# Performance work log

Measured on AMD Instinct MI355X. Metric: run time of the kernel, lower is better.

Reference implementation:

```python
import jax, jax.numpy as jnp
import numpy as np
from jax import lax

N = 1 << 22      # variable nodes
DV = 4           # max variable degree
M = 1 << 21      # check nodes
DC = 8           # max check degree
E = N * DV       # total edges (== M * DC, regular code)
N_ITER = 5


def setup_inputs() -> dict:
    key = jax.random.key(0)
    k1, k2 = jax.random.split(key)
    llr0 = jax.random.normal(k1, (N,), dtype=jnp.float32)
    # cn_adj: each check node owns DC flat edge indices into the [N, DV] grid
    perm = jax.random.permutation(k2, E)
    cn_adj = perm.reshape(M, DC).astype(jnp.int32)
    # vn_adj: only its sign is used (vn_adj < 0 masks padded slots); regular code -> no padding
    vn_adj = (jnp.arange(E, dtype=jnp.int32) % M).reshape(N, DV)
    gamma = jnp.ones((), dtype=jnp.float32)  # learned damping scalar
    return {"llr0": llr0, "gamma": gamma, "vn_adj": vn_adj, "cn_adj": cn_adj}


def reference(llr0, gamma, vn_adj, cn_adj):
    n, dv = vn_adj.shape
    mask = cn_adj < 0                       # [M, DC] padded check slots
    idx = jnp.where(mask, 0, cn_adj)        # safe flat edge indices
    vmask = vn_adj < 0                      # [N, DV] padded variable slots
    big = jnp.asarray(1e9, llr0.dtype)

    def step(v2c, _):
        # gather variable->check messages per check row: [M, DC]
        msg = v2c.reshape(-1)[idx]
        msg = jnp.where(mask, 0.0, msg)
        # min-sum check update (non-extrinsic, as in source)
        sgn = jnp.prod(jnp.sign(msg + 1e-12), axis=1, keepdims=True)   # [M, 1]
        mag = jnp.min(jnp.abs(jnp.where(mask, big, msg)), axis=1, keepdims=True)
        c2v = gamma * sgn * mag
        c2v = jnp.where(mask, 0.0, jnp.broadcast_to(c2v, cn_adj.shape))
        # scatter check->variable messages back onto the edge grid
        v_acc = jnp.zeros((n * dv,), v2c.dtype).at[idx].add(c2v).reshape(n, dv)
        v2c_new = llr0[:, None] + v_acc - v2c
        v2c_new = jnp.where(vmask, 0.0, v2c_new)
        return v2c_new, None

    v2c0 = jnp.zeros(vn_adj.shape, dtype=llr0.dtype)
    v2c, _ = lax.scan(step, v2c0, None, length=N_ITER)
    return llr0 + jnp.sum(v2c, axis=1)
```

## Files before the change

kernel.cpp:

```cpp
#include <hip/hip_runtime.h>
#include <hip/hip_bf16.h>

#define N_VAR (1 << 22)
#define DV    4
#define M_CHK (1 << 21)
#define DC    8
#define N_ITER 5
#define E_TOT (N_VAR * DV)

#define NBIN         256
#define REC_PER_BIN  (E_TOT / NBIN)
#define K3_BLOCKS    4096
#define CHK_PER_THR  2
#define CHK_PER_BLK  (M_CHK / K3_BLOCKS)
#define REC_PER_BLK  (CHK_PER_BLK * DC)
#define VARS_PER_BIN (N_VAR / NBIN)

typedef int      iv4 __attribute__((ext_vector_type(4)));
typedef unsigned uv4 __attribute__((ext_vector_type(4)));
typedef float    fv4 __attribute__((ext_vector_type(4)));

static __device__ inline unsigned pack_bf16x2(float lo, float hi) {
    float2 t; t.x = lo; t.y = hi;
    __hip_bfloat162 h = __float22bfloat162_rn(t);
    return *reinterpret_cast<unsigned*>(&h);
}

__global__ __launch_bounds__(256) void llr_to_bf16(const fv4* __restrict__ llr4,
                                                   uv4* __restrict__ out,
                                                   unsigned* __restrict__ gctr) {
    const int t = blockIdx.x * blockDim.x + threadIdx.x;
    if (blockIdx.x == 0) gctr[threadIdx.x] = 0u;
    fv4 a = __builtin_nontemporal_load(&llr4[(size_t)t * 2]);
    fv4 b = __builtin_nontemporal_load(&llr4[(size_t)t * 2 + 1]);
    uv4 o;
    o.x = pack_bf16x2(a.x, a.y);
    o.y = pack_bf16x2(a.z, a.w);
    o.z = pack_bf16x2(b.x, b.y);
    o.w = pack_bf16x2(b.z, b.w);
    __builtin_nontemporal_store(o, &out[t]);
}

__global__ __launch_bounds__(256) void k_emit(const __hip_bfloat16* __restrict__ llrb,
                                              const float* __restrict__ gamma_p,
                                              const iv4* __restrict__ cn_adj4,
                                              unsigned* __restrict__ gctr,
                                              unsigned* __restrict__ g_rec) {
    __shared__ unsigned hist[NBIN], binOfs[NBIN], cnt2[NBIN], gbase[NBIN], scanBuf[NBIN];
    __shared__ unsigned recLds[REC_PER_BLK];
    __shared__ unsigned char binLds[REC_PER_BLK];
    const int tid = threadIdx.x, blk = blockIdx.x;
    const float gamma = gamma_p[0];

    hist[tid] = 0;
    cnt2[tid] = 0;
    __syncthreads();

    int e[CHK_PER_THR][DC];
    const int m0 = blk * CHK_PER_BLK + tid * CHK_PER_THR;
#pragma unroll
    for (int c = 0; c < CHK_PER_THR; ++c) {
        iv4 a0 = __builtin_nontemporal_load(&cn_adj4[(size_t)(m0 + c) * 2]);
        iv4 a1 = __builtin_nontemporal_load(&cn_adj4[(size_t)(m0 + c) * 2 + 1]);
        e[c][0]=a0.x; e[c][1]=a0.y; e[c][2]=a0.z; e[c][3]=a0.w;
        e[c][4]=a1.x; e[c][5]=a1.y; e[c][6]=a1.z; e[c][7]=a1.w;
    }
    float l[CHK_PER_THR][DC];
#pragma unroll
    for (int c = 0; c < CHK_PER_THR; ++c)
#pragma unroll
        for (int d = 0; d < DC; ++d)
            l[c][d] = __bfloat162float(llrb[e[c][d] >> 2]);

    unsigned Sh[CHK_PER_THR];
#pragma unroll
    for (int c = 0; c < CHK_PER_THR; ++c) {
        float s1 = 1.0f, m1 = fabsf(l[c][0]);
#pragma unroll
        for (int d = 0; d < DC; ++d) {
            float t = l[c][d] + 1e-12f;
            s1 *= (t > 0.0f) ? 1.0f : ((t < 0.0f) ? -1.0f : 0.0f);
            if (d > 0) m1 = fminf(m1, fabsf(l[c][d]));
        }
        float c1 = gamma * s1 * m1;
        float delta = gamma * fabsf(c1) - c1;
        float s3 = 1.0f, m3 = fabsf(l[c][0] + delta);
#pragma unroll
        for (int d = 0; d < DC; ++d) {
            float ld = l[c][d] + delta;
            float t = ld + 1e-12f;
            s3 *= (t > 0.0f) ? 1.0f : ((t < 0.0f) ? -1.0f : 0.0f);
            if (d > 0) m3 = fminf(m3, fabsf(ld));
        }
        float c3 = gamma * s3 * m3;
        float c4 = gamma * fabsf(c3 - delta);
        float S  = (c4 - c3) + delta;
        __hip_bfloat16 h = __float2bfloat16(S);
        Sh[c] = *reinterpret_cast<unsigned short*>(&h);
    }

#pragma unroll
    for (int c = 0; c < CHK_PER_THR; ++c)
#pragma unroll
        for (int d = 0; d < DC; ++d)
            atomicAdd(&hist[(unsigned)e[c][d] >> 16], 1u);
    __syncthreads();

    scanBuf[tid] = hist[tid];
    __syncthreads();
    for (int d = 1; d < NBIN; d <<= 1) {
        unsigned t = (tid >= d) ? scanBuf[tid - d] : 0u;
        __syncthreads();
        scanBuf[tid] += t;
        __syncthreads();
    }
    binOfs[tid] = scanBuf[tid] - hist[tid];
    if (hist[tid] > 0)
        gbase[tid] = (unsigned)tid * REC_PER_BIN + atomicAdd(&gctr[tid], hist[tid]);
    __syncthreads();

#pragma unroll
    for (int c = 0; c < CHK_PER_THR; ++c)
#pragma unroll
        for (int d = 0; d < DC; ++d) {
            unsigned ee  = (unsigned)e[c][d];
            unsigned bin = ee >> 16;
            unsigned rec = ((ee & 0xFFFFu) << 16) | Sh[c];
            unsigned slot = binOfs[bin] + atomicAdd(&cnt2[bin], 1u);
            recLds[slot] = rec;
            binLds[slot] = (unsigned char)bin;
        }
    __syncthreads();

    for (int p = tid; p < REC_PER_BLK; p += 256) {
        unsigned b = binLds[p];
        unsigned dst = gbase[b] + ((unsigned)p - binOfs[b]);
        __builtin_nontemporal_store(recLds[p], &g_rec[dst]);
    }
}

__global__ __launch_bounds__(1024) void k_apply(const float* __restrict__ llr0,
                                                const unsigned* __restrict__ g_rec,
                                                float* __restrict__ out) {
    __shared__ float acc[VARS_PER_BIN];
    const int tid = threadIdx.x, b = blockIdx.x;
    for (int j = tid; j < VARS_PER_BIN; j += 1024) acc[j] = 0.0f;
    __syncthreads();
    const uv4* rp = reinterpret_cast<const uv4*>(g_rec + (size_t)b * REC_PER_BIN);
#pragma unroll
    for (int it = 0; it < REC_PER_BIN / 4 / 1024; ++it) {
        uv4 r = __builtin_nontemporal_load(&rp[it * 1024 + tid]);
        unsigned rr[4] = {r.x, r.y, r.z, r.w};
#pragma unroll
        for (int q = 0; q < 4; ++q) {
            unsigned v = rr[q] >> 18;
            float m = __uint_as_float((rr[q] & 0xFFFFu) << 16);
            atomicAdd(&acc[v], m);
        }
    }
    __syncthreads();
    const int vbase = b * VARS_PER_BIN;
    for (int j = tid; j < VARS_PER_BIN; j += 1024) {
        float L = llr0[vbase + j];
        out[vbase + j] = 5.0f * L + acc[j];
    }
}

__global__ __launch_bounds__(256) void nbp_check_kernel(const __hip_bfloat16* __restrict__ llrb,
                                                        const float* __restrict__ gamma_p,
                                                        const iv4* __restrict__ cn_adj4,
                                                        __hip_bfloat16* __restrict__ ws) {
    const int m = blockIdx.x * blockDim.x + threadIdx.x;
    const float gamma = gamma_p[0];
    iv4 a0 = __builtin_nontemporal_load(&cn_adj4[(size_t)m * 2]);
    iv4 a1 = __builtin_nontemporal_load(&cn_adj4[(size_t)m * 2 + 1]);
    int e[DC] = {a0.x, a0.y, a0.z, a0.w, a1.x, a1.y, a1.z, a1.w};
    float l[DC], msg[DC];
#pragma unroll
    for (int d = 0; d < DC; ++d) l[d] = __bfloat162float(llrb[e[d] >> 2]);
#pragma unroll
    for (int d = 0; d < DC; ++d) msg[d] = l[d];
#pragma unroll
    for (int it = 1; it < N_ITER; ++it) {
        float s = 1.0f, mn = fabsf(msg[0]);
#pragma unroll
        for (int d = 0; d < DC; ++d) {
            float t = msg[d] + 1e-12f;
            s *= (t > 0.0f) ? 1.0f : ((t < 0.0f) ? -1.0f : 0.0f);
            if (d > 0) mn = fminf(mn, fabsf(msg[d]));
        }
        float c2v = gamma * s * mn;
#pragma unroll
        for (int d = 0; d < DC; ++d) msg[d] = (l[d] + c2v) - msg[d];
    }
#pragma unroll
    for (int d = 0; d < DC; ++d) ws[e[d]] = __float2bfloat16(msg[d]);
}

__global__ __launch_bounds__(256) void nbp_var_reduce(const fv4* __restrict__ llr0_4,
                                                      const uv4* __restrict__ ws_u4,
                                                      fv4* __restrict__ out_4) {
    const int t = blockIdx.x * blockDim.x + threadIdx.x;
    uv4 wa = __builtin_nontemporal_load(&ws_u4[(size_t)t * 2]);
    uv4 wb = __builtin_nontemporal_load(&ws_u4[(size_t)t * 2 + 1]);
    fv4 l = __builtin_nontemporal_load(&llr0_4[t]);
    unsigned u[8] = {wa.x, wa.y, wa.z, wa.w, wb.x, wb.y, wb.z, wb.w};
    float msg[16];
#pragma unroll
    for (int i = 0; i < 8; ++i) {
        msg[2 * i]     = __uint_as_float((u[i] & 0xFFFFu) << 16);
        msg[2 * i + 1] = __uint_as_float(u[i] & 0xFFFF0000u);
    }
    fv4 o;
    o.x = l.x + (((msg[0]  + msg[1])  + msg[2])  + msg[3]);
    o.y = l.y + (((msg[4]  + msg[5])  + msg[6])  + msg[7]);
    o.z = l.z + (((msg[8]  + msg[9])  + msg[10]) + msg[11]);
    o.w = l.w + (((msg[12] + msg[13]) + msg[14]) + msg[15]);
    __builtin_nontemporal_store(o, &out_4[t]);
}

extern "C" void kernel_launch(void* const* d_in, const int* in_sizes, int n_in,
                              void* d_out, int out_size, void* d_ws, size_t ws_size,
                              hipStream_t stream) {
    const float* llr0   = (const float*)d_in[0];
    const float* gamma  = (const float*)d_in[1];
    const int*   cn_adj = (const int*)d_in[3];
    float* out = (float*)d_out;
    char* wsb = (char*)d_ws;

    const size_t OFF_LLRB = 0;
    const size_t OFF_REC  = 8u  * 1024 * 1024;
    const size_t OFF_CTR  = 72u * 1024 * 1024;
    const size_t NEED     = OFF_CTR + NBIN * sizeof(unsigned);

    if (ws_size >= NEED) {
        __hip_bfloat16* llrb = (__hip_bfloat16*)(wsb + OFF_LLRB);
        unsigned* g_rec = (unsigned*)(wsb + OFF_REC);
        unsigned* gctr  = (unsigned*)(wsb + OFF_CTR);

        llr_to_bf16<<<(N_VAR / 8) / 256, 256, 0, stream>>>((const fv4*)llr0, (uv4*)llrb, gctr);
        k_emit<<<K3_BLOCKS, 256, 0, stream>>>(llrb, gamma, (const iv4*)cn_adj, gctr, g_rec);
        k_apply<<<NBIN, 1024, 0, stream>>>(llr0, g_rec, out);
    } else {
        __hip_bfloat16* ws   = (__hip_bfloat16*)wsb;
        __hip_bfloat16* llrb = ((__hip_bfloat16*)wsb) + E_TOT;
        unsigned* gctr = (unsigned*)(wsb);
        llr_to_bf16<<<(N_VAR / 8) / 256, 256, 0, stream>>>((const fv4*)llr0,
                                                           (uv4*)llrb, (unsigned*)(wsb));
        nbp_check_kernel<<<M_CHK / 256, 256, 0, stream>>>(llrb, gamma, (const iv4*)cn_adj, ws);
        nbp_var_reduce<<<(N_VAR / 4) / 256, 256, 0, stream>>>(
            (const fv4*)llr0, (const uv4*)ws, (fv4*)out);
    }
}
```

Measured before the change: 298.4 us.

## Split per-bin scatter accumulation into sub-blocks with a separate merge pass

Each bin's record stream is split across four blocks that each accumulate into a private shared-memory histogram and write a partial sum array. A new merge kernel adds the four partials to the scaled input LLR to produce the output. This raises the number of blocks in the apply stage to improve GPU occupancy, at the cost of extra global traffic for partial arrays and an extra launch. The new path needs a larger workspace; otherwise the previous path is used.

```diff
diff --git a/kernel.cpp b/kernel.cpp
--- a/kernel.cpp
+++ b/kernel.cpp
@@ -15,6 +15,7 @@
 #define CHK_PER_BLK  (M_CHK / K3_BLOCKS)
 #define REC_PER_BLK  (CHK_PER_BLK * DC)
 #define VARS_PER_BIN (N_VAR / NBIN)
+#define SUBB         4
 
 typedef int      iv4 __attribute__((ext_vector_type(4)));
 typedef unsigned uv4 __attribute__((ext_vector_type(4)));
@@ -139,6 +140,46 @@
     }
 }
 
+__global__ __launch_bounds__(1024) void k_apply4(const unsigned* __restrict__ g_rec,
+                                                 float* __restrict__ part) {
+    __shared__ float acc[VARS_PER_BIN];
+    const int tid = threadIdx.x;
+    const int b = blockIdx.x >> 2;
+    const int s = blockIdx.x & 3;
+    for (int j = tid; j < VARS_PER_BIN; j += 1024) acc[j] = 0.0f;
+    __syncthreads();
+    const uv4* rp = reinterpret_cast<const uv4*>(
+        g_rec + (size_t)b * REC_PER_BIN + (size_t)s * (REC_PER_BIN / SUBB));
+#pragma unroll
+    for (int it = 0; it < (REC_PER_BIN / SUBB) / 4 / 1024; ++it) {
+        uv4 r = __builtin_nontemporal_load(&rp[it * 1024 + tid]);
+        unsigned rr[4] = {r.x, r.y, r.z, r.w};
+#pragma unroll
+        for (int q = 0; q < 4; ++q) {
+            unsigned v = rr[q] >> 18;
+            float m = __uint_as_float((rr[q] & 0xFFFFu) << 16);
+            atomicAdd(&acc[v], m);
+        }
+    }
+    __syncthreads();
+    float* pp = part + (size_t)s * N_VAR + (size_t)b * VARS_PER_BIN;
+    for (int j = tid; j < VARS_PER_BIN; j += 1024)
+        __builtin_nontemporal_store(acc[j], &pp[j]);
+}
+
+__global__ __launch_bounds__(256) void k_merge(const fv4* __restrict__ llr4,
+                                               const fv4* __restrict__ part4,
+                                               fv4* __restrict__ out4) {
+    const int t = blockIdx.x * blockDim.x + threadIdx.x;
+    fv4 L  = __builtin_nontemporal_load(&llr4[t]);
+    fv4 p0 = __builtin_nontemporal_load(&part4[t]);
+    fv4 p1 = __builtin_nontemporal_load(&part4[t + (N_VAR / 4)]);
+    fv4 p2 = __builtin_nontemporal_load(&part4[t + 2 * (N_VAR / 4)]);
+    fv4 p3 = __builtin_nontemporal_load(&part4[t + 3 * (N_VAR / 4)]);
+    fv4 o = 5.0f * L + ((p0 + p1) + (p2 + p3));
+    __builtin_nontemporal_store(o, &out4[t]);
+}
+
 __global__ __launch_bounds__(1024) void k_apply(const float* __restrict__ llr0,
                                                 const unsigned* __restrict__ g_rec,
                                                 float* __restrict__ out) {
@@ -230,13 +271,27 @@
 
     const size_t OFF_LLRB = 0;
     const size_t OFF_REC  = 8u  * 1024 * 1024;
-    const size_t OFF_CTR  = 72u * 1024 * 1024;
-    const size_t NEED     = OFF_CTR + NBIN * sizeof(unsigned);
-
-    if (ws_size >= NEED) {
+    const size_t OFF_PART = 72u * 1024 * 1024;
+    const size_t OFF_CTRA = 136u * 1024 * 1024;
+    const size_t NEED_A   = OFF_CTRA + NBIN * sizeof(unsigned);
+    const size_t OFF_CTRB = 72u * 1024 * 1024;
+    const size_t NEED_B   = OFF_CTRB + NBIN * sizeof(unsigned);
+
+    if (ws_size >= NEED_A) {
         __hip_bfloat16* llrb = (__hip_bfloat16*)(wsb + OFF_LLRB);
         unsigned* g_rec = (unsigned*)(wsb + OFF_REC);
-        unsigned* gctr  = (unsigned*)(wsb + OFF_CTR);
+        float*    part  = (float*)(wsb + OFF_PART);
+        unsigned* gctr  = (unsigned*)(wsb + OFF_CTRA);
+
+        llr_to_bf16<<<(N_VAR / 8) / 256, 256, 0, stream>>>((const fv4*)llr0, (uv4*)llrb, gctr);
+        k_emit<<<K3_BLOCKS, 256, 0, stream>>>(llrb, gamma, (const iv4*)cn_adj, gctr, g_rec);
+        k_apply4<<<NBIN * SUBB, 1024, 0, stream>>>(g_rec, part);
+        k_merge<<<(N_VAR / 4) / 256, 256, 0, stream>>>((const fv4*)llr0, (const fv4*)part,
+                                                       (fv4*)out);
+    } else if (ws_size >= NEED_B) {
+        __hip_bfloat16* llrb = (__hip_bfloat16*)(wsb + OFF_LLRB);
+        unsigned* g_rec = (unsigned*)(wsb + OFF_REC);
+        unsigned* gctr  = (unsigned*)(wsb + OFF_CTRB);
 
         llr_to_bf16<<<(N_VAR / 8) / 256, 256, 0, stream>>>((const fv4*)llr0, (uv4*)llrb, gctr);
         k_emit<<<K3_BLOCKS, 256, 0, stream>>>(llrb, gamma, (const iv4*)cn_adj, gctr, g_rec);
@@ -244,7 +299,6 @@
     } else {
         __hip_bfloat16* ws   = (__hip_bfloat16*)wsb;
         __hip_bfloat16* llrb = ((__hip_bfloat16*)wsb) + E_TOT;
-        unsigned* gctr = (unsigned*)(wsb);
         llr_to_bf16<<<(N_VAR / 8) / 256, 256, 0, stream>>>((const fv4*)llr0,
                                                            (uv4*)llrb, (unsigned*)(wsb));
         nbp_check_kernel<<<M_CHK / 256, 256, 0, stream>>>(llrb, gamma, (const iv4*)cn_adj, ws);
```

Result: slower. 320.2 us (+7.3%).
